# Optimization experiments

Measured on AMD Instinct MI355X. Metric: run time of the kernel, lower is better.

The kernel has to match this reference:

```python
import jax, jax.numpy as jnp
import numpy as np

# ---- static config (from init_kwargs) ----
B, H, W, C = 4, 256, 256, 96
WS, SS, NH = 8, 4, 3            # window_size, shift_size, num_heads
N = WS * WS                     # tokens per window = 64
NW = (H // WS) * (W // WS)      # windows per image = 1024
HD = C // NH                    # head_dim = 32
SCALE = HD ** -0.5
MLP_H = int(C * 4.0)
EPS = 1e-5


def _relative_position_index():
    coords = np.stack(np.meshgrid(np.arange(WS), np.arange(WS), indexing='ij'))  # (2, WS, WS)
    cf = coords.reshape(2, -1)                       # (2, N)
    rel = (cf[:, :, None] - cf[:, None, :]).transpose(1, 2, 0).astype(np.int64)  # (N, N, 2)
    rel[:, :, 0] += WS - 1
    rel[:, :, 1] += WS - 1
    rel[:, :, 0] *= 2 * WS - 1
    return rel.sum(-1)                               # (N, N) in [0, (2WS-1)^2)


def _attn_mask():
    img = np.zeros((H, W))
    cnt = 0
    slices = (slice(0, -WS), slice(-WS, -SS), slice(-SS, None))
    for hs in slices:
        for ws in slices:
            img[hs, ws] = cnt
            cnt += 1
    m = img.reshape(H // WS, WS, W // WS, WS).transpose(0, 2, 1, 3).reshape(-1, N)  # (NW, N)
    am = m[:, None, :] - m[:, :, None]               # (NW, N, N)
    return np.where(am != 0, -100.0, 0.0).astype(np.float32)


def setup_inputs() -> dict:
    key = jax.random.key(0)
    ks = jax.random.split(key, 8)
    std = 0.02
    inp = {
        'x': jax.random.normal(ks[0], (B, H * W, C), jnp.float32),
        'g1': jnp.ones((C,), jnp.float32),
        'b1': jnp.zeros((C,), jnp.float32),
        'qkv_w': jax.random.normal(ks[1], (3 * C, C), jnp.float32) * std,
        'qkv_b': jnp.zeros((3 * C,), jnp.float32),
        'rpb_table': jax.random.normal(ks[2], ((2 * WS - 1) ** 2, NH), jnp.float32) * std,
        'proj_w': jax.random.normal(ks[3], (C, C), jnp.float32) * std,
        'proj_b': jnp.zeros((C,), jnp.float32),
        'g2': jnp.ones((C,), jnp.float32),
        'b2': jnp.zeros((C,), jnp.float32),
        'fc1_w': jax.random.normal(ks[4], (MLP_H, C), jnp.float32) * std,
        'fc1_b': jnp.zeros((MLP_H,), jnp.float32),
        'fc2_w': jax.random.normal(ks[5], (C, MLP_H), jnp.float32) * std,
        'fc2_b': jnp.zeros((C,), jnp.float32),
        'attn_mask': jnp.asarray(_attn_mask()),
        'rel_index': jnp.asarray(_relative_position_index(), jnp.int32),
    }
    return inp


def _ln(x, g, b):
    mu = jnp.mean(x, -1, keepdims=True)
    var = jnp.mean(jnp.square(x - mu), -1, keepdims=True)
    return (x - mu) * jax.lax.rsqrt(var + EPS) * g + b


def reference(x, g1, b1, qkv_w, qkv_b, rpb_table, proj_w, proj_b,
              g2, b2, fc1_w, fc1_b, fc2_w, fc2_b, attn_mask, rel_index):
    shortcut = x
    h = _ln(x, g1, b1).reshape(B, H, W, C)
    # cyclic shift
    h = jnp.roll(h, (-SS, -SS), axis=(1, 2))
    # window partition -> (B*NW, N, C)
    xw = h.reshape(B, H // WS, WS, W // WS, WS, C).transpose(0, 1, 3, 2, 4, 5).reshape(-1, N, C)
    # qkv projection
    qkv = (xw @ qkv_w.T + qkv_b).reshape(-1, N, 3, NH, HD).transpose(2, 0, 3, 1, 4)  # (3, B_, NH, N, HD)
    q, k, v = qkv[0] * SCALE, qkv[1], qkv[2]
    attn = jnp.einsum('bhnd,bhmd->bhnm', q, k)       # (B_, NH, N, N)
    # gathered relative position bias: (N, N, NH) -> (NH, N, N)
    bias = rpb_table[rel_index].transpose(2, 0, 1)
    attn = attn + bias[None]
    # shifted-window mask
    attn = attn.reshape(B, NW, NH, N, N) + attn_mask[None, :, None]
    attn = jax.nn.softmax(attn.reshape(-1, NH, N, N), axis=-1)
    o = jnp.einsum('bhnm,bhmd->bhnd', attn, v).transpose(0, 2, 1, 3).reshape(-1, N, C)
    o = o @ proj_w.T + proj_b
    # window reverse + reverse shift
    o = o.reshape(B, H // WS, W // WS, WS, WS, C).transpose(0, 1, 3, 2, 4, 5).reshape(B, H, W, C)
    o = jnp.roll(o, (SS, SS), axis=(1, 2)).reshape(B, H * W, C)
    x = shortcut + o
    h2 = _ln(x, g2, b2)
    h2 = jax.nn.gelu(h2 @ fc1_w.T + fc1_b, approximate=False) @ fc2_w.T + fc2_b
    return x + h2
```

## Files before the change

### kernel.cpp

```cpp
#include <hip/hip_runtime.h>
#include <math.h>

constexpr float SCALE_ = 0.17677669529663687f;

typedef float f32x4 __attribute__((ext_vector_type(4)));
typedef short bf16x8 __attribute__((ext_vector_type(8)));
#define MFMA __builtin_amdgcn_mfma_f32_16x16x32_bf16


__device__ inline short f2bf(float f) {
    union { float f; unsigned u; } v; v.f = f;
    unsigned r = v.u + 0x7fffu + ((v.u >> 16) & 1u);
    return (short)(r >> 16);
}
__device__ inline float bf2f(short s) {
    union { unsigned u; float f; } v; v.u = ((unsigned)(unsigned short)s) << 16;
    return v.f;
}
__device__ inline float gelu_erf(float v) {
    float z  = v * 0.70710678118654752f;
    float az = fabsf(z);
    float t  = 1.0f / (1.0f + 0.3275911f * az);
    float p  = t*(0.254829592f + t*(-0.284496736f + t*(1.421413741f +
               t*(-1.453152027f + t*1.061405429f))));
    float er = 1.0f - p * __expf(-az * az);
    return 0.5f * v * (1.0f + copysignf(er, z));
}

__global__ __launch_bounds__(256)
void prep_weights(const float* __restrict__ qkv_w, const float* __restrict__ proj_w,
                  const float* __restrict__ fc1_w, const float* __restrict__ fc2_w,
                  short* __restrict__ ws)
{
    int i = blockIdx.x * 256 + threadIdx.x;
    if (i >= 110592) return;
    float v;
    if      (i < 27648)  v = qkv_w[i];
    else if (i < 36864)  v = proj_w[i - 27648];
    else if (i < 73728)  v = fc1_w[i - 36864];
    else                 v = fc2_w[i - 73728];
    ws[i] = f2bf(v);
}

__global__ __launch_bounds__(256)
void prep_comb(const float* __restrict__ rpb, const int* __restrict__ rel,
               const float* __restrict__ mask, short* __restrict__ comb)
{
    int e = blockIdx.x * 256 + threadIdx.x;
    if (e >= 49152) return;
    int t   = e / 12288;
    int rem = e - t * 12288;
    int h   = rem >> 12;
    int ij  = rem & 4095;
    const int rep[4] = {0, 31, 992, 1023};
    comb[e] = f2bf(rpb[rel[ij] * 3 + h] + mask[(long)rep[t] * 4096 + ij]);
}

__global__ __launch_bounds__(256)
void attn_kernel(const float* __restrict__ x,
                 const float* __restrict__ g1, const float* __restrict__ b1,
                 const short* __restrict__ qkv_wb, const float* __restrict__ qkv_b,
                 const short* __restrict__ proj_wb, const float* __restrict__ proj_b,
                 const short* __restrict__ comb,
                 float* __restrict__ xnew)
{
    __shared__ short aL[64][104];
    __shared__ short qL[64][104];
    __shared__ short kL[64][104];
    __shared__ short vT[96][72];
    __shared__ short pL[64][72];
    __shared__ int   tok_s[64];

    const int tid  = threadIdx.x;
    const int wave = tid >> 6, lane = tid & 63;
    const int lr = lane & 15, lg = lane >> 4;
    const int blk = blockIdx.x;
    const int b = blk >> 10, wi = blk & 1023;
    const int wh = wi >> 5, ww = wi & 31;
    const int mtyp = ((wh == 31) ? 2 : 0) + ((ww == 31) ? 1 : 0);

    if (tid < 64) {
        int r = tid >> 3, c = tid & 7;
        int gh = (wh * 8 + r + 4) & 255;
        int gw = (ww * 8 + c + 4) & 255;
        tok_s[tid] = b * 65536 + gh * 256 + gw;
    }
    __syncthreads();

    {
        const int n = tid >> 2, s = tid & 3;
        const float* xr = x + (long)tok_s[n] * 96 + s * 24;
        float xv[24];
        #pragma unroll
        for (int i = 0; i < 6; i++) {
            float4 t = ((const float4*)xr)[i];
            xv[4*i]=t.x; xv[4*i+1]=t.y; xv[4*i+2]=t.z; xv[4*i+3]=t.w;
        }
        float s1 = 0.f, s2 = 0.f;
        #pragma unroll
        for (int i = 0; i < 24; i++) { s1 += xv[i]; s2 += xv[i]*xv[i]; }
        s1 += __shfl_xor(s1, 1); s2 += __shfl_xor(s2, 1);
        s1 += __shfl_xor(s1, 2); s2 += __shfl_xor(s2, 2);
        float mu = s1 * (1.0f/96.0f);
        float var = s2 * (1.0f/96.0f) - mu*mu;
        float rs = rsqrtf(var + 1e-5f);
        #pragma unroll
        for (int c = 0; c < 24; c++)
            aL[n][s*24+c] = f2bf((xv[c]-mu)*rs*g1[s*24+c] + b1[s*24+c]);
    }
    __syncthreads();

    {
        const int wm = wave >> 1, wn = wave & 1;
        bf16x8 afr[2][3];
        #pragma unroll
        for (int mt = 0; mt < 2; mt++)
            #pragma unroll
            for (int kt = 0; kt < 3; kt++)
                afr[mt][kt] = *(const bf16x8*)&aL[(2*wm+mt)*16 + lr][kt*32 + lg*8];
        for (int nt0 = 0; nt0 < 9; nt0++) {
            const int nt = wn * 9 + nt0;
            const int o  = nt * 16 + lr;
            bf16x8 bfr[3];
            #pragma unroll
            for (int kt = 0; kt < 3; kt++)
                bfr[kt] = *(const bf16x8*)&qkv_wb[(long)o * 96 + kt*32 + lg*8];
            const float bias = qkv_b[o];
            #pragma unroll
            for (int mt = 0; mt < 2; mt++) {
                f32x4 acc = {bias, bias, bias, bias};
                #pragma unroll
                for (int kt = 0; kt < 3; kt++)
                    acc = MFMA(afr[mt][kt], bfr[kt], acc, 0, 0, 0);
                const int row0 = (2*wm+mt)*16 + lg*4;
                if (nt < 6) {
                    #pragma unroll
                    for (int r = 0; r < 4; r++) qL[row0+r][o] = f2bf(acc[r]*SCALE_);
                } else if (nt < 12) {
                    #pragma unroll
                    for (int r = 0; r < 4; r++) kL[row0+r][o-96] = f2bf(acc[r]);
                } else {
                    #pragma unroll
                    for (int r = 0; r < 4; r++) vT[o-192][row0+r] = f2bf(acc[r]);
                }
            }
        }
    }
    __syncthreads();

    for (int h = 0; h < 3; h++) {
        const short* cb = comb + (mtyp * 3 + h) * 4096;
        bf16x8 qf = *(const bf16x8*)&qL[wave*16 + lr][h*32 + lg*8];
        float sv[4][4];
        #pragma unroll
        for (int nt = 0; nt < 4; nt++) {
            bf16x8 kf = *(const bf16x8*)&kL[nt*16 + lr][h*32 + lg*8];
            f32x4 s = MFMA(qf, kf, (f32x4){0.f,0.f,0.f,0.f}, 0, 0, 0);
            #pragma unroll
            for (int r = 0; r < 4; r++) {
                int i = wave*16 + lg*4 + r;
                int j = nt*16 + lr;
                sv[nt][r] = s[r] + bf2f(cb[i*64 + j]);
            }
        }
        float mx[4], sm[4];
        #pragma unroll
        for (int r = 0; r < 4; r++) {
            mx[r] = fmaxf(fmaxf(sv[0][r], sv[1][r]), fmaxf(sv[2][r], sv[3][r]));
            mx[r] = fmaxf(mx[r], __shfl_xor(mx[r], 1));
            mx[r] = fmaxf(mx[r], __shfl_xor(mx[r], 2));
            mx[r] = fmaxf(mx[r], __shfl_xor(mx[r], 4));
            mx[r] = fmaxf(mx[r], __shfl_xor(mx[r], 8));
            sm[r] = 0.f;
        }
        #pragma unroll
        for (int nt = 0; nt < 4; nt++)
            #pragma unroll
            for (int r = 0; r < 4; r++) { sv[nt][r] = __expf(sv[nt][r]-mx[r]); sm[r] += sv[nt][r]; }
        #pragma unroll
        for (int r = 0; r < 4; r++) {
            sm[r] += __shfl_xor(sm[r], 1);
            sm[r] += __shfl_xor(sm[r], 2);
            sm[r] += __shfl_xor(sm[r], 4);
            sm[r] += __shfl_xor(sm[r], 8);
            sm[r] = 1.0f / sm[r];
        }
        #pragma unroll
        for (int nt = 0; nt < 4; nt++)
            #pragma unroll
            for (int r = 0; r < 4; r++)
                pL[wave*16 + lg*4 + r][nt*16 + lr] = f2bf(sv[nt][r]*sm[r]);

        bf16x8 pf[2];
        #pragma unroll
        for (int kt = 0; kt < 2; kt++)
            pf[kt] = *(const bf16x8*)&pL[wave*16 + lr][kt*32 + lg*8];
        #pragma unroll
        for (int nt = 0; nt < 2; nt++) {
            f32x4 acc = {0.f,0.f,0.f,0.f};
            #pragma unroll
            for (int kt = 0; kt < 2; kt++) {
                bf16x8 vf = *(const bf16x8*)&vT[h*32 + nt*16 + lr][kt*32 + lg*8];
                acc = MFMA(pf[kt], vf, acc, 0, 0, 0);
            }
            #pragma unroll
            for (int r = 0; r < 4; r++)
                aL[wave*16 + lg*4 + r][h*32 + nt*16 + lr] = f2bf(acc[r]);
        }
    }
    __syncthreads();

    {
        const int wm = wave >> 1, wn = wave & 1;
        bf16x8 afr[2][3];
        #pragma unroll
        for (int mt = 0; mt < 2; mt++)
            #pragma unroll
            for (int kt = 0; kt < 3; kt++)
                afr[mt][kt] = *(const bf16x8*)&aL[(2*wm+mt)*16 + lr][kt*32 + lg*8];
        for (int nt0 = 0; nt0 < 3; nt0++) {
            const int nt = wn * 3 + nt0;
            const int c  = nt * 16 + lr;
            bf16x8 bfr[3];
            #pragma unroll
            for (int kt = 0; kt < 3; kt++)
                bfr[kt] = *(const bf16x8*)&proj_wb[(long)c * 96 + kt*32 + lg*8];
            const float bias = proj_b[c];
            #pragma unroll
            for (int mt = 0; mt < 2; mt++) {
                f32x4 acc = {bias, bias, bias, bias};
                #pragma unroll
                for (int kt = 0; kt < 3; kt++)
                    acc = MFMA(afr[mt][kt], bfr[kt], acc, 0, 0, 0);
                #pragma unroll
                for (int r = 0; r < 4; r++) {
                    int i = (2*wm+mt)*16 + lg*4 + r;
                    long ad = (long)tok_s[i] * 96 + c;
                    xnew[ad] = acc[r] + x[ad];
                }
            }
        }
    }
}

__global__ __launch_bounds__(256)
void mlp_kernel(const float* __restrict__ g2, const float* __restrict__ b2,
                const short* __restrict__ fc1_wb, const float* __restrict__ fc1_b,
                const short* __restrict__ fc2_wb, const float* __restrict__ fc2_b,
                float* __restrict__ xio)
{
    __shared__ short aL[64][104];
    __shared__ short hch[64][72];
    const int tid  = threadIdx.x;
    const int wave = tid >> 6, lane = tid & 63;
    const int lr = lane & 15, lg = lane >> 4;
    const int wm = wave >> 1, wn = wave & 1;
    const long base = (long)blockIdx.x * 6144;

    {
        const int n = tid >> 2, s = tid & 3;
        const float* xr = xio + base + n * 96 + s * 24;
        float xv[24];
        #pragma unroll
        for (int i = 0; i < 6; i++) {
            float4 t = ((const float4*)xr)[i];
            xv[4*i]=t.x; xv[4*i+1]=t.y; xv[4*i+2]=t.z; xv[4*i+3]=t.w;
        }
        float s1 = 0.f, s2 = 0.f;
        #pragma unroll
        for (int i = 0; i < 24; i++) { s1 += xv[i]; s2 += xv[i]*xv[i]; }
        s1 += __shfl_xor(s1, 1); s2 += __shfl_xor(s2, 1);
        s1 += __shfl_xor(s1, 2); s2 += __shfl_xor(s2, 2);
        float mu = s1 * (1.0f/96.0f);
        float var = s2 * (1.0f/96.0f) - mu*mu;
        float rs = rsqrtf(var + 1e-5f);
        #pragma unroll
        for (int c = 0; c < 24; c++)
            aL[n][s*24+c] = f2bf((xv[c]-mu)*rs*g2[s*24+c] + b2[s*24+c]);
    }
    __syncthreads();

    bf16x8 afr[2][3];
    #pragma unroll
    for (int mt = 0; mt < 2; mt++)
        #pragma unroll
        for (int kt = 0; kt < 3; kt++)
            afr[mt][kt] = *(const bf16x8*)&aL[(2*wm+mt)*16 + lr][kt*32 + lg*8];

    f32x4 facc[2][3];
    #pragma unroll
    for (int nt = 0; nt < 3; nt++) {
        const float bias = fc2_b[wn*48 + nt*16 + lr];
        facc[0][nt] = (f32x4){bias, bias, bias, bias};
        facc[1][nt] = facc[0][nt];
    }

    for (int c = 0; c < 6; c++) {
        #pragma unroll
        for (int nt = 0; nt < 2; nt++) {
            const int oc = wn*32 + nt*16 + lr;
            const int o  = c*64 + oc;
            bf16x8 bfr[3];
            #pragma unroll
            for (int kt = 0; kt < 3; kt++)
                bfr[kt] = *(const bf16x8*)&fc1_wb[(long)o * 96 + kt*32 + lg*8];
            const float bias = fc1_b[o];
            #pragma unroll
            for (int mt = 0; mt < 2; mt++) {
                f32x4 acc = {bias, bias, bias, bias};
                #pragma unroll
                for (int kt = 0; kt < 3; kt++)
                    acc = MFMA(afr[mt][kt], bfr[kt], acc, 0, 0, 0);
                const int row0 = (2*wm+mt)*16 + lg*4;
                #pragma unroll
                for (int r = 0; r < 4; r++)
                    hch[row0+r][oc] = f2bf(gelu_erf(acc[r]));
            }
        }
        __syncthreads();
        #pragma unroll
        for (int mt = 0; mt < 2; mt++) {
            bf16x8 a0 = *(const bf16x8*)&hch[(2*wm+mt)*16 + lr][lg*8];
            bf16x8 a1 = *(const bf16x8*)&hch[(2*wm+mt)*16 + lr][32 + lg*8];
            #pragma unroll
            for (int nt = 0; nt < 3; nt++) {
                const int c2 = wn*48 + nt*16 + lr;
                bf16x8 b0 = *(const bf16x8*)&fc2_wb[(long)c2 * 384 + c*64 + lg*8];
                bf16x8 b1 = *(const bf16x8*)&fc2_wb[(long)c2 * 384 + c*64 + 32 + lg*8];
                facc[mt][nt] = MFMA(a0, b0, facc[mt][nt], 0, 0, 0);
                facc[mt][nt] = MFMA(a1, b1, facc[mt][nt], 0, 0, 0);
            }
        }
        __syncthreads();
    }

    #pragma unroll
    for (int mt = 0; mt < 2; mt++)
        #pragma unroll
        for (int nt = 0; nt < 3; nt++) {
            const int c2 = wn*48 + nt*16 + lr;
            #pragma unroll
            for (int r = 0; r < 4; r++) {
                int i = (2*wm+mt)*16 + lg*4 + r;
                long ad = base + (long)i * 96 + c2;
                xio[ad] = facc[mt][nt][r] + xio[ad];
            }
        }
}

extern "C" void kernel_launch(void* const* d_in, const int* in_sizes, int n_in,
                              void* d_out, int out_size, void* d_ws, size_t ws_size,
                              hipStream_t stream)
{
    const float* x      = (const float*)d_in[0];
    const float* g1     = (const float*)d_in[1];
    const float* b1     = (const float*)d_in[2];
    const float* qkv_w  = (const float*)d_in[3];
    const float* qkv_b  = (const float*)d_in[4];
    const float* rpb    = (const float*)d_in[5];
    const float* proj_w = (const float*)d_in[6];
    const float* proj_b = (const float*)d_in[7];
    const float* g2     = (const float*)d_in[8];
    const float* b2     = (const float*)d_in[9];
    const float* fc1_w  = (const float*)d_in[10];
    const float* fc1_b  = (const float*)d_in[11];
    const float* fc2_w  = (const float*)d_in[12];
    const float* fc2_b  = (const float*)d_in[13];
    const float* mask   = (const float*)d_in[14];
    const int*   rel    = (const int*)d_in[15];
    float* out = (float*)d_out;

    short* wsS    = (short*)d_ws;
    short* qkv_wb = wsS;
    short* proj_wb= wsS + 27648;
    short* fc1_wb = wsS + 36864;
    short* fc2_wb = wsS + 73728;
    short* comb   = wsS + 110592;

    prep_weights<<<432, 256, 0, stream>>>(qkv_w, proj_w, fc1_w, fc2_w, wsS);
    prep_comb<<<192, 256, 0, stream>>>(rpb, rel, mask, comb);
    attn_kernel<<<4096, 256, 0, stream>>>(x, g1, b1, qkv_wb, qkv_b,
                                          proj_wb, proj_b, comb, out);
    mlp_kernel<<<4096, 256, 0, stream>>>(g2, b2, fc1_wb, fc1_b, fc2_wb, fc2_b, out);
}
```

Before: 264.3 us.

## Double-buffer MLP hidden chunk, prefetch fc1 weights, use fast reciprocal in GELU

The MLP kernel now double-buffers the hidden-activation shared tile, which lets it drop the second barrier in each chunk iteration. It also prefetches the next chunk's fc1 weights and bias into registers while the current chunk's results go through GELU. The GELU reciprocal becomes the hardware rcp builtin, and launch bounds request 4 blocks per CU. The extra register-held weights and larger LDS footprint may cut occupancy, and the approximate reciprocal slightly changes numerics.

```diff
diff --git a/kernel.cpp b/kernel.cpp
--- a/kernel.cpp
+++ b/kernel.cpp
@@ -20,7 +20,7 @@
 __device__ inline float gelu_erf(float v) {
     float z  = v * 0.70710678118654752f;
     float az = fabsf(z);
-    float t  = 1.0f / (1.0f + 0.3275911f * az);
+    float t  = __builtin_amdgcn_rcpf(1.0f + 0.3275911f * az);
     float p  = t*(0.254829592f + t*(-0.284496736f + t*(1.421413741f +
                t*(-1.453152027f + t*1.061405429f))));
     float er = 1.0f - p * __expf(-az * az);
@@ -243,14 +243,14 @@
     }
 }
 
-__global__ __launch_bounds__(256)
+__global__ __launch_bounds__(256, 4)
 void mlp_kernel(const float* __restrict__ g2, const float* __restrict__ b2,
                 const short* __restrict__ fc1_wb, const float* __restrict__ fc1_b,
                 const short* __restrict__ fc2_wb, const float* __restrict__ fc2_b,
                 float* __restrict__ xio)
 {
     __shared__ short aL[64][104];
-    __shared__ short hch[64][72];
+    __shared__ short hch[2][64][72];
     const int tid  = threadIdx.x;
     const int wave = tid >> 6, lane = tid & 63;
     const int lr = lane & 15, lg = lane >> 4;
@@ -295,43 +295,65 @@
         facc[1][nt] = facc[0][nt];
     }
 
+    bf16x8 bfrA[2][3];
+    float  biasA[2];
+    #pragma unroll
+    for (int nt = 0; nt < 2; nt++) {
+        const int o = wn*32 + nt*16 + lr;
+        #pragma unroll
+        for (int kt = 0; kt < 3; kt++)
+            bfrA[nt][kt] = *(const bf16x8*)&fc1_wb[(long)o * 96 + kt*32 + lg*8];
+        biasA[nt] = fc1_b[o];
+    }
+
     for (int c = 0; c < 6; c++) {
+        const int cb = c & 1;
+        f32x4 acc1[2][2];
+        #pragma unroll
+        for (int nt = 0; nt < 2; nt++)
+            #pragma unroll
+            for (int mt = 0; mt < 2; mt++) {
+                f32x4 acc = {biasA[nt], biasA[nt], biasA[nt], biasA[nt]};
+                #pragma unroll
+                for (int kt = 0; kt < 3; kt++)
+                    acc = MFMA(afr[mt][kt], bfrA[nt][kt], acc, 0, 0, 0);
+                acc1[nt][mt] = acc;
+            }
+        if (c < 5) {
+            #pragma unroll
+            for (int nt = 0; nt < 2; nt++) {
+                const int o = (c+1)*64 + wn*32 + nt*16 + lr;
+                #pragma unroll
+                for (int kt = 0; kt < 3; kt++)
+                    bfrA[nt][kt] = *(const bf16x8*)&fc1_wb[(long)o * 96 + kt*32 + lg*8];
+                biasA[nt] = fc1_b[o];
+            }
+        }
         #pragma unroll
         for (int nt = 0; nt < 2; nt++) {
             const int oc = wn*32 + nt*16 + lr;
-            const int o  = c*64 + oc;
-            bf16x8 bfr[3];
-            #pragma unroll
-            for (int kt = 0; kt < 3; kt++)
-                bfr[kt] = *(const bf16x8*)&fc1_wb[(long)o * 96 + kt*32 + lg*8];
-            const float bias = fc1_b[o];
             #pragma unroll
             for (int mt = 0; mt < 2; mt++) {
-                f32x4 acc = {bias, bias, bias, bias};
-                #pragma unroll
-                for (int kt = 0; kt < 3; kt++)
-                    acc = MFMA(afr[mt][kt], bfr[kt], acc, 0, 0, 0);
                 const int row0 = (2*wm+mt)*16 + lg*4;
                 #pragma unroll
                 for (int r = 0; r < 4; r++)
-                    hch[row0+r][oc] = f2bf(gelu_erf(acc[r]));
+                    hch[cb][row0+r][oc] = f2bf(gelu_erf(acc1[nt][mt][r]));
             }
         }
         __syncthreads();
         #pragma unroll
         for (int mt = 0; mt < 2; mt++) {
-            bf16x8 a0 = *(const bf16x8*)&hch[(2*wm+mt)*16 + lr][lg*8];
-            bf16x8 a1 = *(const bf16x8*)&hch[(2*wm+mt)*16 + lr][32 + lg*8];
+            bf16x8 a0 = *(const bf16x8*)&hch[cb][(2*wm+mt)*16 + lr][lg*8];
+            bf16x8 a1 = *(const bf16x8*)&hch[cb][(2*wm+mt)*16 + lr][32 + lg*8];
             #pragma unroll
             for (int nt = 0; nt < 3; nt++) {
-                const int c2 = wn*48 + nt*16 + lr;
-                bf16x8 b0 = *(const bf16x8*)&fc2_wb[(long)c2 * 384 + c*64 + lg*8];
-                bf16x8 b1 = *(const bf16x8*)&fc2_wb[(long)c2 * 384 + c*64 + 32 + lg*8];
+                const long wb = (long)(wn*48 + nt*16 + lr) * 384 + c*64;
+                bf16x8 b0 = *(const bf16x8*)&fc2_wb[wb + lg*8];
+                bf16x8 b1 = *(const bf16x8*)&fc2_wb[wb + 32 + lg*8];
                 facc[mt][nt] = MFMA(a0, b0, facc[mt][nt], 0, 0, 0);
                 facc[mt][nt] = MFMA(a1, b1, facc[mt][nt], 0, 0, 0);
             }
         }
-        __syncthreads();
     }
 
     #pragma unroll
```

New measurement: 242.4 us. 8.3% less time.
